# Performance work log

Hardware: AMD Instinct MI355X
Metric: run time of the kernel (lower is better)

## Reference

```python
import jax, jax.numpy as jnp
import numpy as np

NUM_HEADS = 16
NUM_KV_HEADS = 4
ROPE_BASE = 10000.0
TRAIN_SEQ_LEN = 1024


def _rms_norm(x):
    eps = jnp.finfo(x.dtype).eps
    var = jnp.mean(jnp.square(x), axis=-1, keepdims=True)
    return x * jax.lax.rsqrt(var + eps)


def _rotary_cos_sin(seq_len, head_dim, dtype):
    # NTK-by-parts base scaling when seq_len > train_seq_len (matches Rotary.forward)
    if seq_len > TRAIN_SEQ_LEN:
        scale = seq_len / TRAIN_SEQ_LEN
        base = ROPE_BASE * scale ** (head_dim / (head_dim - 2))
    else:
        base = ROPE_BASE
    inv_freq = 1.0 / base ** (jnp.arange(0, head_dim, 2, dtype=jnp.float32) / head_dim)
    t = jnp.arange(seq_len, dtype=jnp.float32)
    freqs = jnp.outer(t, inv_freq)  # [S, head_dim//2]
    return jnp.cos(freqs).astype(dtype), jnp.sin(freqs).astype(dtype)


def _apply_rotary(x, cos, sin):
    # x: [B,S,H,D]; cos/sin: [S, D//2] broadcast over batch and heads
    half = x.shape[-1] // 2
    x1, x2 = x[..., :half], x[..., half:]
    c = cos[None, :, None, :]
    s = sin[None, :, None, :]
    return jnp.concatenate((x1 * c + x2 * s, -x1 * s + x2 * c), axis=-1)


def setup_inputs() -> dict:
    key = jax.random.key(0)
    ks = jax.random.split(key, 5)
    B, S, D = 2, 2048, 2048
    KVD = NUM_KV_HEADS * (D // NUM_HEADS)
    x = jax.random.normal(ks[0], (B, S, D), dtype=jnp.float32)
    Wq = jax.random.normal(ks[1], (D, D), dtype=jnp.float32) * 0.02
    Wk = jax.random.normal(ks[2], (KVD, D), dtype=jnp.float32) * 0.02
    Wv = jax.random.normal(ks[3], (KVD, D), dtype=jnp.float32) * 0.02
    Wproj = jax.random.normal(ks[4], (D, D), dtype=jnp.float32) * 0.02
    q_gain = jnp.ones((NUM_HEADS,), dtype=jnp.float32)
    return {"x": x, "Wq": Wq, "Wk": Wk, "Wv": Wv, "Wproj": Wproj, "q_gain": q_gain}


def reference(x, Wq, Wk, Wv, Wproj, q_gain):
    B, S, D = x.shape
    H, KH = NUM_HEADS, NUM_KV_HEADS
    hd = D // H
    group = H // KH

    q = (x @ Wq.T).reshape(B, S, H, hd)
    k = (x @ Wk.T).reshape(B, S, KH, hd)
    v = (x @ Wv.T).reshape(B, S, KH, hd)

    q = _rms_norm(q)
    k = _rms_norm(k)

    cos, sin = _rotary_cos_sin(S, hd, q.dtype)
    q = _apply_rotary(q, cos, sin)
    k = _apply_rotary(k, cos, sin)

    q = q * q_gain.astype(q.dtype)[None, None, :, None]

    # GQA: query head h attends to kv head h // group
    k = jnp.repeat(k, group, axis=2)  # [B,S,H,hd]
    v = jnp.repeat(v, group, axis=2)

    scale = 1.0 / jnp.sqrt(jnp.asarray(hd, dtype=q.dtype))
    scores = jnp.einsum("bshd,bthd->bhst", q, k) * scale  # [B,H,S,S]
    causal = jnp.tril(jnp.ones((S, S), dtype=bool))
    scores = jnp.where(causal[None, None], scores, jnp.asarray(-jnp.inf, scores.dtype))
    probs = jax.nn.softmax(scores, axis=-1)
    out = jnp.einsum("bhst,bthd->bshd", probs, v)  # [B,S,H,hd]

    return out.reshape(B, S, D) @ Wproj.T
```

## Files before the change

kernel.cpp:

```cpp
#include <hip/hip_runtime.h>
#include <cmath>

typedef unsigned short u16;
typedef short v8s __attribute__((ext_vector_type(8)));
typedef float v4f __attribute__((ext_vector_type(4)));
typedef unsigned short v4u __attribute__((ext_vector_type(4)));
typedef unsigned int v2u __attribute__((ext_vector_type(2)));

__device__ __forceinline__ u16 f2bf(float f) {
  unsigned u = __builtin_bit_cast(unsigned, f);
  u += 0x7fffu + ((u >> 16) & 1u);
  return (u16)(u >> 16);
}
__device__ __forceinline__ float bf2f(u16 h) {
  unsigned u = ((unsigned)h) << 16;
  return __builtin_bit_cast(float, u);
}
__device__ __forceinline__ unsigned pk2(float a, float b) {
  return (unsigned)f2bf(a) | ((unsigned)f2bf(b) << 16);
}

__global__ void k_cast_bf16(const float* __restrict__ in, u16* __restrict__ out, int n4) {
  int i = blockIdx.x * blockDim.x + threadIdx.x;
  if (i >= n4) return;
  v4f v = ((const v4f*)in)[i];
  v4u o;
  o[0] = f2bf(v[0]); o[1] = f2bf(v[1]); o[2] = f2bf(v[2]); o[3] = f2bf(v[3]);
  ((v4u*)out)[i] = o;
}

__global__ void k_cast_w(const float* __restrict__ a, const float* __restrict__ b,
                         const float* __restrict__ c, const float* __restrict__ d,
                         u16* __restrict__ oa, u16* __restrict__ ob, u16* __restrict__ oc,
                         u16* __restrict__ od, int na4, int nb4, int nc4, int nd4) {
  int j = blockIdx.x * blockDim.x + threadIdx.x;
  const float* src;
  u16* dst;
  if (j < na4) { src = a; dst = oa; }
  else {
    j -= na4;
    if (j < nb4) { src = b; dst = ob; }
    else {
      j -= nb4;
      if (j < nc4) { src = c; dst = oc; }
      else {
        j -= nc4;
        if (j >= nd4) return;
        src = d; dst = od;
      }
    }
  }
  v4f v = ((const v4f*)src)[j];
  v4u o;
  o[0] = f2bf(v[0]); o[1] = f2bf(v[1]); o[2] = f2bf(v[2]); o[3] = f2bf(v[3]);
  ((v4u*)dst)[j] = o;
}

__global__ void k_rope_tab(float* __restrict__ cosT, float* __restrict__ sinT, float log2_base) {
  int idx = blockIdx.x * blockDim.x + threadIdx.x;
  int t = idx >> 6, i = idx & 63;
  float inv = exp2f(-(float)i * (1.0f / 64.0f) * log2_base);
  float fr = (float)t * inv;
  cosT[idx] = cosf(fr);
  sinT[idx] = sinf(fr);
}

__global__ void k_rmsnorm_rope(u16* __restrict__ qk, const float* __restrict__ cosT,
                               const float* __restrict__ sinT, const float* __restrict__ gain,
                               int H, int S, float oscale) {
  int row = blockIdx.x * 4 + (threadIdx.x >> 6);
  int l = threadIdx.x & 63;
  int h = row % H;
  int m = row / H;
  int s = m % S;
  u16* p = qk + (size_t)row * 128;
  float a = bf2f(p[l]), b = bf2f(p[64 + l]);
  float ss = a * a + b * b;
#pragma unroll
  for (int o = 32; o; o >>= 1) ss += __shfl_xor(ss, o, 64);
  float r = rsqrtf(ss * (1.0f / 128.0f) + 1.1920929e-7f);
  a *= r; b *= r;
  float c = cosT[s * 64 + l], sn = sinT[s * 64 + l];
  float o1 = a * c + b * sn;
  float o2 = b * c - a * sn;
  float g = oscale;
  if (gain != nullptr) g *= gain[h];
  p[l] = f2bf(o1 * g);
  p[64 + l] = f2bf(o2 * g);
}

__device__ __forceinline__ void stage8(char* sL, const u16* __restrict__ Ag,
                                       const u16* __restrict__ Bg, int row0, int col0, int K,
                                       int n, int NT2, int tid) {
  int tile = n >> 2;
  if (tile >= NT2) return;
  int part = n & 3;
  int isB = part & 1;
  int half = (part == 1 || part == 2) ? 1 : 0;
  int k0 = tile * 64;
  if (!isB) {
    char* base = sL + (tile & 1) * 65536 + half * 8192;
    int o = tid * 16;
    int rowp = o >> 8;
    int un = (o & 255) ^ ((rowp & 15) << 4);
    int rsub = rowp + ((un >> 7) << 5);
    int k = (un & 127) >> 1;
    const u16* src = Ag + (size_t)(row0 + half * 64 + rsub) * K + (k0 + k);
    __builtin_amdgcn_global_load_lds((const __attribute__((address_space(1))) void*)src,
                                     (__attribute__((address_space(3))) void*)(base + o), 16, 0, 0);
  } else {
    char* base = sL + (tile & 1) * 65536 + 16384 + half * 24576;
#pragma unroll
    for (int j = 0; j < 3; ++j) {
      int o = (j * 512 + tid) * 16;
      int rowp = o >> 8;
      int un = (o & 255) ^ ((rowp & 15) << 4);
      int rsub = rowp + (un >> 7) * 96;
      int k = (un & 127) >> 1;
      const u16* src = Bg + (size_t)(col0 + half * 192 + rsub) * K + (k0 + k);
      __builtin_amdgcn_global_load_lds((const __attribute__((address_space(1))) void*)src,
                                       (__attribute__((address_space(3))) void*)(base + o), 16, 0,
                                       0);
    }
  }
}

#define PH(BUF, MH, NH, LA, LB, WAITC)                                                            \
  {                                                                                               \
    if (LA) {                                                                                     \
      _Pragma("unroll") for (int mi = 0; mi < 2; ++mi) {                                          \
        _Pragma("unroll") for (int c = 0; c < 2; ++c) {                                           \
          af[mi][c] = *(const v8s*)(sL + (BUF)*65536 + (MH)*8192 + (mi * 16 + lr) * 256 +         \
                                    ((wm * 128 + c * 64 + lh * 16) ^ (lr << 4)));                 \
        }                                                                                         \
      }                                                                                           \
    }                                                                                             \
    if (LB) {                                                                                     \
      _Pragma("unroll") for (int ni = 0; ni < 3; ++ni) {                                          \
        _Pragma("unroll") for (int c = 0; c < 2; ++c) {                                           \
          bf[ni][c] = *(const v8s*)(sL + (BUF)*65536 + 16384 + (NH)*24576 +                       \
                                    ((wn & 1) * 48 + ni * 16 + lr) * 256 +                        \
                                    (((wn >> 1) * 128 + c * 64 + lh * 16) ^ (lr << 4)));          \
        }                                                                                         \
      }                                                                                           \
    }                                                                                             \
    stage8(sL, Ag, Bg, row0, col0, K, n, NT2, tid);                                               \
    ++n;                                                                                          \
    if (WAITC) {                                                                                  \
      if (((n - 1) >> 2) < NT2) asm volatile("s_waitcnt vmcnt(4)" ::: "memory");                  \
      else asm volatile("s_waitcnt vmcnt(0)" ::: "memory");                                       \
    }                                                                                             \
    __builtin_amdgcn_sched_barrier(0);                                                            \
    __builtin_amdgcn_s_barrier();                                                                 \
    asm volatile("s_waitcnt lgkmcnt(0)" ::: "memory");                                            \
    __builtin_amdgcn_sched_barrier(0);                                                            \
    __builtin_amdgcn_s_setprio(1);                                                                \
    _Pragma("unroll") for (int mi = 0; mi < 2; ++mi) {                                            \
      _Pragma("unroll") for (int ni = 0; ni < 3; ++ni) {                                          \
        _Pragma("unroll") for (int c = 0; c < 2; ++c) {                                           \
          acc[(MH)*2 + mi][(NH)*3 + ni] = __builtin_amdgcn_mfma_f32_16x16x32_bf16(                \
              af[mi][c], bf[ni][c], acc[(MH)*2 + mi][(NH)*3 + ni], 0, 0, 0);                      \
        }                                                                                         \
      }                                                                                           \
    }                                                                                             \
    __builtin_amdgcn_s_setprio(0);                                                                \
    __builtin_amdgcn_sched_barrier(0);                                                            \
    __builtin_amdgcn_s_barrier();                                                                 \
  }

__global__ __launch_bounds__(512, 2) void k_gemm_qkv8(const u16* __restrict__ Ag,
                                                      const u16* __restrict__ Bg,
                                                      u16* __restrict__ q_o, u16* __restrict__ k_o,
                                                      u16* __restrict__ v_o, int M, int K) {
  __shared__ char sL[131072];
  const int tid = threadIdx.x;
  const int wid = tid >> 6, l = tid & 63;
  const int lr = l & 15, lh = l >> 4;
  const int wm = wid >> 2, wn = wid & 3;
  const int nwg = gridDim.x * gridDim.y;
  const int bid = blockIdx.y * gridDim.x + blockIdx.x;
  const int cpx = nwg >> 3;
  const int swz = (bid & 7) * cpx + (bid >> 3);
  const int row0 = (swz / gridDim.x) * 128, col0 = (swz % gridDim.x) * 384;
  const int NT2 = K >> 6;

  v4f zz = {0.f, 0.f, 0.f, 0.f};
  v4f acc[4][6];
#pragma unroll
  for (int i = 0; i < 4; ++i)
#pragma unroll
    for (int j = 0; j < 6; ++j) acc[i][j] = zz;
  v8s af[2][2], bf[3][2];

  for (int i = 0; i < 6; ++i) stage8(sL, Ag, Bg, row0, col0, K, i, NT2, tid);
  asm volatile("s_waitcnt vmcnt(4)" ::: "memory");
  __builtin_amdgcn_sched_barrier(0);
  __builtin_amdgcn_s_barrier();

  int n = 6;
  for (int it = 0; it < NT2 / 2; ++it) {
    PH(0, 0, 0, 1, 1, 0)
    PH(0, 0, 1, 0, 1, 0)
    PH(0, 1, 1, 1, 0, 0)
    PH(0, 1, 0, 0, 1, 1)
    PH(1, 0, 0, 1, 1, 0)
    PH(1, 0, 1, 0, 1, 0)
    PH(1, 1, 1, 1, 0, 0)
    PH(1, 1, 0, 0, 1, 1)
  }

#pragma unroll
  for (int MH = 0; MH < 2; ++MH) {
#pragma unroll
    for (int mi = 0; mi < 2; ++mi) {
#pragma unroll
      for (int NH = 0; NH < 2; ++NH) {
#pragma unroll
        for (int ni = 0; ni < 3; ++ni) {
          int row = row0 + MH * 64 + wm * 32 + mi * 16 + lh * 4;
          int col = col0 + NH * 192 + wn * 48 + ni * 16 + lr;
          v4f a_ = acc[MH * 2 + mi][NH * 3 + ni];
          if (col < 2048) {
#pragma unroll
            for (int r = 0; r < 4; ++r) q_o[(size_t)(row + r) * 2048 + col] = f2bf(a_[r]);
          } else if (col < 2560) {
#pragma unroll
            for (int r = 0; r < 4; ++r) k_o[(size_t)(row + r) * 512 + (col - 2048)] = f2bf(a_[r]);
          } else {
#pragma unroll
            for (int r = 0; r < 4; ++r) v_o[(size_t)(col - 2560) * M + row + r] = f2bf(a_[r]);
          }
        }
      }
    }
  }
}

__global__ __launch_bounds__(256) void k_gemm_bt(const u16* __restrict__ A,
                                                 const u16* __restrict__ Bw,
                                                 float* __restrict__ C, int M, int N, int K) {
  __shared__ u16 sA[128 * 32];
  __shared__ u16 sB[128 * 32];
  const int tid = threadIdx.x;
  const int w = tid >> 6, l = tid & 63;
  const int lr = l & 15, lh = l >> 4;
  const int wr = w >> 1, wc = w & 1;
  const int nwg = gridDim.x * gridDim.y;
  const int bid = blockIdx.y * gridDim.x + blockIdx.x;
  const int cpx = nwg >> 3;
  const int swz = (bid & 7) * cpx + (bid >> 3);
  const int row0 = (swz / gridDim.x) * 128, col0 = (swz % gridDim.x) * 128;
  v4f zz = {0.f, 0.f, 0.f, 0.f};
  v4f acc[4][4];
#pragma unroll
  for (int mi = 0; mi < 4; ++mi)
#pragma unroll
    for (int ni = 0; ni < 4; ++ni) acc[mi][ni] = zz;

  const int lrow = l >> 2;
  const int lcol = (l & 3) * 8;

  for (int k0 = 0; k0 < K; k0 += 32) {
#pragma unroll
    for (int i = 0; i < 2; ++i) {
      int c = i * 4 + w;
      const u16* srcA = A + (size_t)(row0 + c * 16 + lrow) * K + (k0 + lcol);
      const u16* srcB = Bw + (size_t)(col0 + c * 16 + lrow) * K + (k0 + lcol);
      __builtin_amdgcn_global_load_lds((const __attribute__((address_space(1))) void*)srcA,
                                       (__attribute__((address_space(3))) void*)(sA + c * 512),
                                       16, 0, 0);
      __builtin_amdgcn_global_load_lds((const __attribute__((address_space(1))) void*)srcB,
                                       (__attribute__((address_space(3))) void*)(sB + c * 512),
                                       16, 0, 0);
    }
    __syncthreads();
    v8s af[4], bfr[4];
#pragma unroll
    for (int mi = 0; mi < 4; ++mi)
      af[mi] = *(const v8s*)(sA + (wr * 64 + mi * 16 + lr) * 32 + lh * 8);
#pragma unroll
    for (int ni = 0; ni < 4; ++ni)
      bfr[ni] = *(const v8s*)(sB + (wc * 64 + ni * 16 + lr) * 32 + lh * 8);
#pragma unroll
    for (int mi = 0; mi < 4; ++mi)
#pragma unroll
      for (int ni = 0; ni < 4; ++ni)
        acc[mi][ni] = __builtin_amdgcn_mfma_f32_16x16x32_bf16(af[mi], bfr[ni], acc[mi][ni], 0, 0, 0);
    __syncthreads();
  }
#pragma unroll
  for (int mi = 0; mi < 4; ++mi) {
#pragma unroll
    for (int ni = 0; ni < 4; ++ni) {
      int row = row0 + wr * 64 + mi * 16 + lh * 4;
      int col = col0 + wc * 64 + ni * 16 + lr;
#pragma unroll
      for (int r = 0; r < 4; ++r) C[(size_t)(row + r) * N + col] = acc[mi][ni][r];
    }
  }
}

__global__ __launch_bounds__(256) void k_flash_attn(const u16* __restrict__ Q,
                                                    const u16* __restrict__ Kb,
                                                    const u16* __restrict__ Vt,
                                                    u16* __restrict__ O, int S, int H, int KH,
                                                    int Mtot) {
  const int bh = blockIdx.x;
  const int h = bh % H, b = bh / H;
  const int kvh = h / (H / KH);
  const int w = threadIdx.x >> 6, l = threadIdx.x & 63;
  const int lr = l & 15, lh = l >> 4;

  __shared__ alignas(16) char sK[2][16384];
  __shared__ alignas(16) char sV[2][16384];
  __shared__ alignas(16) unsigned P_lds[4][16 * 32];
  unsigned* prow = P_lds[w] + lr * 32;
  const int xr = (lr & 7) << 2;

  v4f zz = {0.f, 0.f, 0.f, 0.f};
  const int strideK = KH * 128;
  const int strideKB = strideK * 2;
  const char* KheadB = (const char*)Kb + 2 * ((size_t)b * S * strideK + (size_t)kvh * 128);
  const char* VheadB = (const char*)Vt + 2 * ((size_t)(kvh * 128) * Mtot + (size_t)b * S);
  const size_t MtotB = (size_t)Mtot * 2;

  auto stage = [&](int kv0, int bufi) {
    const char* Kt = KheadB + (size_t)kv0 * strideKB;
#pragma unroll
    for (int j = 0; j < 4; ++j) {
      int jj = w * 4 + j;
      int ci = jj * 64 + l;
      int r = ci >> 4;
      int bc = (ci & 15) << 4;
      const char* src = Kt + (size_t)r * strideKB + (bc ^ ((r & 15) << 4));
      __builtin_amdgcn_global_load_lds((const __attribute__((address_space(1))) void*)src,
                                       (__attribute__((address_space(3))) void*)(sK[bufi] + jj * 1024),
                                       16, 0, 0);
    }
    const char* Vt0 = VheadB + (size_t)kv0 * 2;
#pragma unroll
    for (int j = 0; j < 4; ++j) {
      int jj = w * 4 + j;
      int ci = jj * 64 + l;
      int r = ci >> 3;
      int bc = (ci & 7) << 4;
      const char* src = Vt0 + (size_t)r * MtotB + (bc ^ ((r & 7) << 4));
      __builtin_amdgcn_global_load_lds((const __attribute__((address_space(1))) void*)src,
                                       (__attribute__((address_space(3))) void*)(sV[bufi] + jj * 1024),
                                       16, 0, 0);
    }
  };

  for (int pp = 0; pp < 2; ++pp) {
    const int qt = (pp == 0) ? (int)blockIdx.y : (S / 64 - 1 - (int)blockIdx.y);
    const int q0 = qt * 64;
    const int nt = qt + 1;
    const int qi = q0 + w * 16 + lr;

    v8s qf[4];
    const u16* qp = Q + (size_t)(b * S + q0 + w * 16 + lr) * (size_t)(H * 128) + h * 128 + lh * 8;
#pragma unroll
    for (int c = 0; c < 4; ++c) qf[c] = *(const v8s*)(qp + c * 32);

    v4f o_acc[8];
#pragma unroll
    for (int df = 0; df < 8; ++df) o_acc[df] = zz;
    float m_run = -1e30f, l_run = 0.f;

    stage(0, 0);
    __syncthreads();

    int buf = 0;
    for (int t = 0; t < nt; ++t) {
      const int kv0 = t * 64;
      const bool lastTile = (t == nt - 1);
      const char* sKb = sK[buf];
      const char* sVb = sV[buf];

      v4f sv[4];
      __builtin_amdgcn_s_setprio(1);
#pragma unroll
      for (int nf = 0; nf < 4; ++nf) {
        v4f a_ = zz;
        const int r = nf * 16 + lr;
#pragma unroll
        for (int c = 0; c < 4; ++c) {
          v8s kf = *(const v8s*)(sKb + r * 256 + ((lh * 16 + c * 64) ^ (lr << 4)));
          a_ = __builtin_amdgcn_mfma_f32_16x16x32_bf16(kf, qf[c], a_, 0, 0, 0);
        }
        sv[nf] = a_;
      }
      __builtin_amdgcn_s_setprio(0);

      if (t + 1 < nt) stage(kv0 + 64, buf ^ 1);

      if (lastTile) {
#pragma unroll
        for (int nf = 0; nf < 4; ++nf)
#pragma unroll
          for (int r = 0; r < 4; ++r)
            if (kv0 + nf * 16 + lh * 4 + r > qi) sv[nf][r] = -1e30f;
      }
      float pmax = -1e30f;
#pragma unroll
      for (int nf = 0; nf < 4; ++nf)
#pragma unroll
        for (int r = 0; r < 4; ++r) pmax = fmaxf(pmax, sv[nf][r]);
      pmax = fmaxf(pmax, __shfl_xor(pmax, 16, 64));
      pmax = fmaxf(pmax, __shfl_xor(pmax, 32, 64));
      if (!__all(pmax - m_run <= 8.0f)) {
        float mnew = fmaxf(m_run, pmax);
        float corr = exp2f(m_run - mnew);
        l_run *= corr;
        m_run = mnew;
        float corrq[4];
#pragma unroll
        for (int r = 0; r < 4; ++r) corrq[r] = __shfl(corr, lh * 4 + r, 16);
#pragma unroll
        for (int df = 0; df < 8; ++df)
#pragma unroll
          for (int r = 0; r < 4; ++r) o_acc[df][r] *= corrq[r];
      }
      float rsum = 0.f;
#pragma unroll
      for (int nf = 0; nf < 4; ++nf)
#pragma unroll
        for (int r = 0; r < 4; ++r) {
          float pv = exp2f(sv[nf][r] - m_run);
          sv[nf][r] = pv;
          rsum += pv;
        }
      rsum += __shfl_xor(rsum, 16, 64);
      rsum += __shfl_xor(rsum, 32, 64);
      l_run += rsum;

#pragma unroll
      for (int nf = 0; nf < 4; ++nf) {
        v2u pw;
        pw[0] = pk2(sv[nf][0], sv[nf][1]);
        pw[1] = pk2(sv[nf][2], sv[nf][3]);
        *(v2u*)(prow + ((nf * 8 + lh * 2) ^ xr)) = pw;
      }
      asm volatile("s_waitcnt lgkmcnt(0)" ::: "memory");
      __builtin_amdgcn_sched_barrier(0);
      v8s ap[2];
#pragma unroll
      for (int c2 = 0; c2 < 2; ++c2) ap[c2] = *(const v8s*)(prow + ((c2 * 16 + lh * 4) ^ xr));

      __builtin_amdgcn_s_setprio(1);
#pragma unroll
      for (int df = 0; df < 8; ++df) {
        const int r = df * 16 + lr;
        const char* vrow = sVb + r * 128;
        const int key = (lr & 7) << 4;
#pragma unroll
        for (int c2 = 0; c2 < 2; ++c2) {
          v8s vf = *(const v8s*)(vrow + ((lh * 16 + c2 * 64) ^ key));
          o_acc[df] = __builtin_amdgcn_mfma_f32_16x16x32_bf16(ap[c2], vf, o_acc[df], 0, 0, 0);
        }
      }
      __builtin_amdgcn_s_setprio(0);

      __syncthreads();
      buf ^= 1;
    }

    float rl = 1.0f / l_run;
    float invq[4];
#pragma unroll
    for (int r = 0; r < 4; ++r) invq[r] = __shfl(rl, lh * 4 + r, 16);
    u16* op = O + (size_t)(b * S + q0 + w * 16 + lh * 4) * (size_t)(H * 128) + h * 128;
#pragma unroll
    for (int r = 0; r < 4; ++r)
#pragma unroll
      for (int df = 0; df < 8; ++df)
        op[(size_t)r * (H * 128) + df * 16 + lr] = f2bf(o_acc[df][r] * invq[r]);
  }
}

extern "C" void kernel_launch(void* const* d_in, const int* in_sizes, int n_in, void* d_out,
                              int out_size, void* d_ws, size_t ws_size, hipStream_t stream) {
  const float* x = (const float*)d_in[0];
  const float* Wq = (const float*)d_in[1];
  const float* Wk = (const float*)d_in[2];
  const float* Wv = (const float*)d_in[3];
  const float* Wp = (const float*)d_in[4];
  const float* gain = (const float*)d_in[5];
  float* out = (float*)d_out;

  const int B = 2, S = 2048, D = 2048, H = 16, KH = 4;
  const int M = B * S;
  const int KVD = KH * 128;
  const int NQKV = D + 2 * KVD;

  char* w = (char*)d_ws;
  u16* x_bf = (u16*)w;   w += (size_t)M * D * 2;
  u16* wqkv = (u16*)w;   w += (size_t)NQKV * D * 2;
  u16* wp_bf = (u16*)w;  w += (size_t)D * D * 2;
  u16* q_bf = (u16*)w;   w += (size_t)M * D * 2;
  u16* k_bf = (u16*)w;   w += (size_t)M * KVD * 2;
  u16* v_t = (u16*)w;    w += (size_t)M * KVD * 2;
  u16* ao_bf = (u16*)w;  w += (size_t)M * D * 2;
  float* cosT = (float*)w; w += (size_t)S * 64 * 4;
  float* sinT = (float*)w; w += (size_t)S * 64 * 4;
  if ((size_t)(w - (char*)d_ws) > ws_size) return;

  k_cast_bf16<<<(M * D / 4 + 255) / 256, 256, 0, stream>>>(x, x_bf, M * D / 4);
  {
    int na4 = D * D / 4, nb4 = KVD * D / 4, nc4 = KVD * D / 4, nd4 = D * D / 4;
    int tot = na4 + nb4 + nc4 + nd4;
    k_cast_w<<<(tot + 255) / 256, 256, 0, stream>>>(
        Wq, Wk, Wv, Wp, wqkv, wqkv + (size_t)D * D, wqkv + (size_t)(D + KVD) * D, wp_bf,
        na4, nb4, nc4, nd4);
  }

  double scale = (double)S / 1024.0;
  double base = (S > 1024) ? 10000.0 * pow(scale, 128.0 / 126.0) : 10000.0;
  float l2b = (float)(log(base) / log(2.0));
  k_rope_tab<<<S * 64 / 256, 256, 0, stream>>>(cosT, sinT, l2b);

  dim3 gqkv(NQKV / 384, M / 128);
  k_gemm_qkv8<<<gqkv, 512, 0, stream>>>(x_bf, wqkv, q_bf, k_bf, v_t, M, D);

  float qscale = 1.4426950408889634f / sqrtf(128.0f);
  k_rmsnorm_rope<<<(M * H) / 4, 256, 0, stream>>>(q_bf, cosT, sinT, gain, H, S, qscale);
  k_rmsnorm_rope<<<(M * KH) / 4, 256, 0, stream>>>(k_bf, cosT, sinT, nullptr, KH, S, 1.0f);

  dim3 blk(256);
  dim3 ga(B * H, S / 128);
  k_flash_attn<<<ga, blk, 0, stream>>>(q_bf, k_bf, v_t, ao_bf, S, H, KH, M);

  dim3 gp(D / 128, M / 128);
  k_gemm_bt<<<gp, blk, 0, stream>>>(ao_bf, wp_bf, out, M, D, D);
}
```

Measured before the change: 225.1 us.

## Replace output projection GEMM with 8-wave pipelined 128x256 tile kernel

Replaces the simple single-buffered 128x128 output-projection GEMM with a 512-thread kernel that computes 128x256 tiles. It double-buffers K=64 slabs in swizzled LDS, interleaves partial-tile staging with MFMA phases under explicit vmcnt waits and barriers, and raises MFMA priority. The aim is to overlap global loads with compute and reduce per-step synchronization stalls that the old kernel paid on every K=32 step. It also switches bf16 packing to the hardware v_cvt_pk_bf16_f32 instruction and restructures the softmax max reduction as a tree. The tradeoffs are 96KB of LDS per block, which limits occupancy, and a fragile hand-written wait-count schedule.

```diff
diff --git a/kernel.cpp b/kernel.cpp
--- a/kernel.cpp
+++ b/kernel.cpp
@@ -17,7 +17,9 @@
   return __builtin_bit_cast(float, u);
 }
 __device__ __forceinline__ unsigned pk2(float a, float b) {
-  return (unsigned)f2bf(a) | ((unsigned)f2bf(b) << 16);
+  unsigned r;
+  asm("v_cvt_pk_bf16_f32 %0, %1, %2" : "=v"(r) : "v"(a), "v"(b));
+  return r;
 }
 
 __global__ void k_cast_bf16(const float* __restrict__ in, u16* __restrict__ out, int n4) {
@@ -236,66 +238,140 @@
   }
 }
 
-__global__ __launch_bounds__(256) void k_gemm_bt(const u16* __restrict__ A,
-                                                 const u16* __restrict__ Bw,
-                                                 float* __restrict__ C, int M, int N, int K) {
-  __shared__ u16 sA[128 * 32];
-  __shared__ u16 sB[128 * 32];
+__device__ __forceinline__ void stage8b(char* sL, const u16* __restrict__ Ag,
+                                        const u16* __restrict__ Bg, int row0, int col0, int K,
+                                        int n, int NT2, int tid) {
+  int tile = n >> 2;
+  if (tile >= NT2) return;
+  int part = n & 3;
+  int isB = part & 1;
+  int half = (part == 1 || part == 2) ? 1 : 0;
+  int k0 = tile * 64;
+  if (!isB) {
+    char* base = sL + (tile & 1) * 49152 + half * 8192;
+    int o = tid * 16;
+    int rowp = o >> 8;
+    int un = (o & 255) ^ ((rowp & 15) << 4);
+    int rsub = rowp + ((un >> 7) << 5);
+    int k = (un & 127) >> 1;
+    const u16* src = Ag + (size_t)(row0 + half * 64 + rsub) * K + (k0 + k);
+    __builtin_amdgcn_global_load_lds((const __attribute__((address_space(1))) void*)src,
+                                     (__attribute__((address_space(3))) void*)(base + o), 16, 0, 0);
+  } else {
+    char* base = sL + (tile & 1) * 49152 + 16384 + half * 16384;
+#pragma unroll
+    for (int j = 0; j < 2; ++j) {
+      int o = (j * 512 + tid) * 16;
+      int rowp = o >> 8;
+      int un = (o & 255) ^ ((rowp & 15) << 4);
+      int rsub = rowp + (un >> 7) * 64;
+      int k = (un & 127) >> 1;
+      const u16* src = Bg + (size_t)(col0 + half * 128 + rsub) * K + (k0 + k);
+      __builtin_amdgcn_global_load_lds((const __attribute__((address_space(1))) void*)src,
+                                       (__attribute__((address_space(3))) void*)(base + o), 16, 0,
+                                       0);
+    }
+  }
+}
+
+#define PH2(BUF, MH, NH, LA, LB, WAITC)                                                           \
+  {                                                                                               \
+    if (LA) {                                                                                     \
+      _Pragma("unroll") for (int mi = 0; mi < 2; ++mi) {                                          \
+        _Pragma("unroll") for (int c = 0; c < 2; ++c) {                                           \
+          af[mi][c] = *(const v8s*)(sL + (BUF)*49152 + (MH)*8192 + (mi * 16 + lr) * 256 +         \
+                                    ((wm * 128 + c * 64 + lh * 16) ^ (lr << 4)));                 \
+        }                                                                                         \
+      }                                                                                           \
+    }                                                                                             \
+    if (LB) {                                                                                     \
+      _Pragma("unroll") for (int ni = 0; ni < 2; ++ni) {                                          \
+        _Pragma("unroll") for (int c = 0; c < 2; ++c) {                                           \
+          bf[ni][c] = *(const v8s*)(sL + (BUF)*49152 + 16384 + (NH)*16384 +                       \
+                                    ((wn & 1) * 32 + ni * 16 + lr) * 256 +                        \
+                                    (((wn >> 1) * 128 + c * 64 + lh * 16) ^ (lr << 4)));          \
+        }                                                                                         \
+      }                                                                                           \
+    }                                                                                             \
+    stage8b(sL, Ag, Bg, row0, col0, K, n, NT2, tid);                                              \
+    ++n;                                                                                          \
+    if (WAITC) {                                                                                  \
+      if (((n - 1) >> 2) < NT2) asm volatile("s_waitcnt vmcnt(3)" ::: "memory");                  \
+      else asm volatile("s_waitcnt vmcnt(0)" ::: "memory");                                       \
+    }                                                                                             \
+    __builtin_amdgcn_sched_barrier(0);                                                            \
+    __builtin_amdgcn_s_barrier();                                                                 \
+    asm volatile("s_waitcnt lgkmcnt(0)" ::: "memory");                                            \
+    __builtin_amdgcn_sched_barrier(0);                                                            \
+    __builtin_amdgcn_s_setprio(1);                                                                \
+    _Pragma("unroll") for (int mi = 0; mi < 2; ++mi) {                                            \
+      _Pragma("unroll") for (int ni = 0; ni < 2; ++ni) {                                          \
+        _Pragma("unroll") for (int c = 0; c < 2; ++c) {                                           \
+          acc[(MH)*2 + mi][(NH)*2 + ni] = __builtin_amdgcn_mfma_f32_16x16x32_bf16(                \
+              af[mi][c], bf[ni][c], acc[(MH)*2 + mi][(NH)*2 + ni], 0, 0, 0);                      \
+        }                                                                                         \
+      }                                                                                           \
+    }                                                                                             \
+    __builtin_amdgcn_s_setprio(0);                                                                \
+    __builtin_amdgcn_sched_barrier(0);                                                            \
+    __builtin_amdgcn_s_barrier();                                                                 \
+  }
+
+__global__ __launch_bounds__(512, 2) void k_gemm_bt8(const u16* __restrict__ Ag,
+                                                     const u16* __restrict__ Bg,
+                                                     float* __restrict__ C, int M, int N, int K) {
+  __shared__ char sL[98304];
   const int tid = threadIdx.x;
-  const int w = tid >> 6, l = tid & 63;
+  const int wid = tid >> 6, l = tid & 63;
   const int lr = l & 15, lh = l >> 4;
-  const int wr = w >> 1, wc = w & 1;
+  const int wm = wid >> 2, wn = wid & 3;
   const int nwg = gridDim.x * gridDim.y;
   const int bid = blockIdx.y * gridDim.x + blockIdx.x;
   const int cpx = nwg >> 3;
   const int swz = (bid & 7) * cpx + (bid >> 3);
-  const int row0 = (swz / gridDim.x) * 128, col0 = (swz % gridDim.x) * 128;
+  const int row0 = (swz / gridDim.x) * 128, col0 = (swz % gridDim.x) * 256;
+  const int NT2 = K >> 6;
+
   v4f zz = {0.f, 0.f, 0.f, 0.f};
   v4f acc[4][4];
 #pragma unroll
-  for (int mi = 0; mi < 4; ++mi)
-#pragma unroll
-    for (int ni = 0; ni < 4; ++ni) acc[mi][ni] = zz;
-
-  const int lrow = l >> 2;
-  const int lcol = (l & 3) * 8;
-
-  for (int k0 = 0; k0 < K; k0 += 32) {
-#pragma unroll
-    for (int i = 0; i < 2; ++i) {
-      int c = i * 4 + w;
-      const u16* srcA = A + (size_t)(row0 + c * 16 + lrow) * K + (k0 + lcol);
-      const u16* srcB = Bw + (size_t)(col0 + c * 16 + lrow) * K + (k0 + lcol);
-      __builtin_amdgcn_global_load_lds((const __attribute__((address_space(1))) void*)srcA,
-                                       (__attribute__((address_space(3))) void*)(sA + c * 512),
-                                       16, 0, 0);
-      __builtin_amdgcn_global_load_lds((const __attribute__((address_space(1))) void*)srcB,
-                                       (__attribute__((address_space(3))) void*)(sB + c * 512),
-                                       16, 0, 0);
-    }
-    __syncthreads();
-    v8s af[4], bfr[4];
-#pragma unroll
-    for (int mi = 0; mi < 4; ++mi)
-      af[mi] = *(const v8s*)(sA + (wr * 64 + mi * 16 + lr) * 32 + lh * 8);
-#pragma unroll
-    for (int ni = 0; ni < 4; ++ni)
-      bfr[ni] = *(const v8s*)(sB + (wc * 64 + ni * 16 + lr) * 32 + lh * 8);
-#pragma unroll
-    for (int mi = 0; mi < 4; ++mi)
-#pragma unroll
-      for (int ni = 0; ni < 4; ++ni)
-        acc[mi][ni] = __builtin_amdgcn_mfma_f32_16x16x32_bf16(af[mi], bfr[ni], acc[mi][ni], 0, 0, 0);
-    __syncthreads();
-  }
-#pragma unroll
-  for (int mi = 0; mi < 4; ++mi) {
-#pragma unroll
-    for (int ni = 0; ni < 4; ++ni) {
-      int row = row0 + wr * 64 + mi * 16 + lh * 4;
-      int col = col0 + wc * 64 + ni * 16 + lr;
-#pragma unroll
-      for (int r = 0; r < 4; ++r) C[(size_t)(row + r) * N + col] = acc[mi][ni][r];
+  for (int i = 0; i < 4; ++i)
+#pragma unroll
+    for (int j = 0; j < 4; ++j) acc[i][j] = zz;
+  v8s af[2][2], bf[2][2];
+
+  for (int i = 0; i < 6; ++i) stage8b(sL, Ag, Bg, row0, col0, K, i, NT2, tid);
+  asm volatile("s_waitcnt vmcnt(3)" ::: "memory");
+  __builtin_amdgcn_sched_barrier(0);
+  __builtin_amdgcn_s_barrier();
+
+  int n = 6;
+  for (int it = 0; it < NT2 / 2; ++it) {
+    PH2(0, 0, 0, 1, 1, 0)
+    PH2(0, 0, 1, 0, 1, 0)
+    PH2(0, 1, 1, 1, 0, 0)
+    PH2(0, 1, 0, 0, 1, 1)
+    PH2(1, 0, 0, 1, 1, 0)
+    PH2(1, 0, 1, 0, 1, 0)
+    PH2(1, 1, 1, 1, 0, 0)
+    PH2(1, 1, 0, 0, 1, 1)
+  }
+
+#pragma unroll
+  for (int MH = 0; MH < 2; ++MH) {
+#pragma unroll
+    for (int mi = 0; mi < 2; ++mi) {
+#pragma unroll
+      for (int NH = 0; NH < 2; ++NH) {
+#pragma unroll
+        for (int ni = 0; ni < 2; ++ni) {
+          int row = row0 + MH * 64 + wm * 32 + mi * 16 + lh * 4;
+          int col = col0 + NH * 128 + (wn & 1) * 32 + (wn >> 1) * 64 + ni * 16 + lr;
+          v4f a_ = acc[MH * 2 + mi][NH * 2 + ni];
+#pragma unroll
+          for (int r = 0; r < 4; ++r) C[(size_t)(row + r) * N + col] = a_[r];
+        }
+      }
     }
   }
 }
@@ -401,11 +477,11 @@
           for (int r = 0; r < 4; ++r)
             if (kv0 + nf * 16 + lh * 4 + r > qi) sv[nf][r] = -1e30f;
       }
-      float pmax = -1e30f;
-#pragma unroll
-      for (int nf = 0; nf < 4; ++nf)
-#pragma unroll
-        for (int r = 0; r < 4; ++r) pmax = fmaxf(pmax, sv[nf][r]);
+      float pm0 = fmaxf(fmaxf(sv[0][0], sv[0][1]), fmaxf(sv[0][2], sv[0][3]));
+      float pm1 = fmaxf(fmaxf(sv[1][0], sv[1][1]), fmaxf(sv[1][2], sv[1][3]));
+      float pm2 = fmaxf(fmaxf(sv[2][0], sv[2][1]), fmaxf(sv[2][2], sv[2][3]));
+      float pm3 = fmaxf(fmaxf(sv[3][0], sv[3][1]), fmaxf(sv[3][2], sv[3][3]));
+      float pmax = fmaxf(fmaxf(pm0, pm1), fmaxf(pm2, pm3));
       pmax = fmaxf(pmax, __shfl_xor(pmax, 16, 64));
       pmax = fmaxf(pmax, __shfl_xor(pmax, 32, 64));
       if (!__all(pmax - m_run <= 8.0f)) {
@@ -530,6 +606,6 @@
   dim3 ga(B * H, S / 128);
   k_flash_attn<<<ga, blk, 0, stream>>>(q_bf, k_bf, v_t, ao_bf, S, H, KH, M);
 
-  dim3 gp(D / 128, M / 128);
-  k_gemm_bt<<<gp, blk, 0, stream>>>(ao_bf, wp_bf, out, M, D, D);
-}
+  dim3 gp(D / 256, M / 128);
+  k_gemm_bt8<<<gp, 512, 0, stream>>>(ao_bf, wp_bf, out, M, D, D);
+}
```

Result: faster. 208.2 us (-7.5%).
